# Performance work log

Hardware: AMD Instinct MI355X
Metric: run time of the kernel (lower is better)

## Reference

```python
import jax, jax.numpy as jnp
import numpy as np

V, E, H = 50000, 256, 512
BS, SEQ = 64, 200


def setup_inputs() -> dict:
    key = jax.random.key(0)
    ks = jax.random.split(key, 16)
    s = 0.05
    return {
        "input_idx": jax.random.randint(ks[0], (BS,), 0, V),
        "encoded": jax.random.normal(ks[1], (BS, SEQ, 2 * H), jnp.float32),
        "encoded_idx": jax.random.randint(ks[2], (BS, SEQ), 0, V),
        "prev_state": jax.random.normal(ks[3], (BS, H), jnp.float32),
        "weighted": jax.random.normal(ks[4], (BS, 1, 2 * H), jnp.float32),
        "order": 1,
        "embed_W": jax.random.normal(ks[5], (V, E), jnp.float32) * s,
        "Wih": jax.random.normal(ks[6], (3 * H, E + 2 * H), jnp.float32) * s,
        "Whh": jax.random.normal(ks[7], (3 * H, H), jnp.float32) * s,
        "bih": jax.random.normal(ks[8], (3 * H,), jnp.float32) * s,
        "bhh": jax.random.normal(ks[9], (3 * H,), jnp.float32) * s,
        "Ws_W": jax.random.normal(ks[10], (H, 2 * H), jnp.float32) * s,
        "Ws_b": jax.random.normal(ks[11], (H,), jnp.float32) * s,
        "Wo_W": jax.random.normal(ks[12], (V, H), jnp.float32) * s,
        "Wo_b": jax.random.normal(ks[13], (V,), jnp.float32) * s,
        "Wc_W": jax.random.normal(ks[14], (H, 2 * H), jnp.float32) * s,
        "Wc_b": jax.random.normal(ks[15], (H,), jnp.float32) * s,
    }


def reference(input_idx, encoded, encoded_idx, prev_state, weighted, order,
              embed_W, Wih, Whh, bih, bhh, Ws_W, Ws_b, Wo_W, Wo_b, Wc_W, Wc_b):
    bs, seq, _ = encoded.shape
    hidden = Ws_W.shape[0]
    vocab = Wo_W.shape[0]

    if order == 0:
        prev_state = encoded[:, 1] @ Ws_W.T + Ws_b            # [bs, H]
        weighted = jnp.zeros((bs, 1, 2 * hidden), encoded.dtype)

    # GRU single step (batch_first, seq len 1)
    x = jnp.concatenate([embed_W[input_idx], weighted[:, 0, :]], axis=1)  # [bs, E+2H]
    gi = x @ Wih.T + bih                                       # [bs, 3H]
    gh = prev_state @ Whh.T + bhh                              # [bs, 3H]
    i_r, i_z, i_n = jnp.split(gi, 3, axis=1)
    h_r, h_z, h_n = jnp.split(gh, 3, axis=1)
    r = jax.nn.sigmoid(i_r + h_r)
    z = jax.nn.sigmoid(i_z + h_z)
    n = jnp.tanh(i_n + r * h_n)
    state = (1.0 - z) * n + z * prev_state                     # [bs, H]

    # generate and copy scores
    score_g = state @ Wo_W.T + Wo_b                            # [bs, V]
    sc = jnp.tanh(encoded @ Wc_W.T + Wc_b)                     # [bs, seq, H]
    score_c = jnp.einsum('bsh,bh->bs', sc, state)              # [bs, seq]
    enc_mask = jnp.where(encoded_idx == 0, -1000.0, 0.0).astype(score_c.dtype)
    score_c = jnp.tanh(score_c + enc_mask)

    probs = jax.nn.softmax(jnp.concatenate([score_g, score_c], axis=1), axis=1)
    prob_g = probs[:, :vocab]                                  # [bs, V]
    prob_c = probs[:, vocab:]                                  # [bs, seq]

    # scatter-add copy probs into vocab slots
    prob_c_to_g = jnp.zeros((bs, vocab), probs.dtype).at[
        jnp.arange(bs)[:, None], encoded_idx].add(prob_c)
    out = (prob_g + prob_c_to_g)[:, None, :]                   # [bs, 1, V]

    # selective-read attention over positions matching input token
    m = (encoded_idx == input_idx[:, None]).astype(encoded.dtype)  # [bs, seq]
    ssum = m.sum(axis=1, keepdims=True)
    m = jnp.where(ssum > 1, m / ssum, m)
    attn = (prob_c * m)[:, None, :]                            # [bs, 1, seq]
    weighted_out = attn @ encoded                              # [bs, 1, 2H]

    return out, state, weighted_out
```

## Files before the change

kernel.cpp:

```cpp
#include <hip/hip_runtime.h>

#define V 50000
#define E_DIM 256
#define H_DIM 512
#define H2 1024
#define G3 1536
#define BSZ 64
#define SEQ 200
#define KX 1280
#define MROWS 12800
#define NBLK_WO 782

#define XBF_OFF   0
#define H0_OFF    40960
#define H0BF_OFF  73728
#define GI_OFF    90112
#define GH_OFF    188416
#define STBF_OFF  286720
#define WCBF_OFF  303104
#define SC_OFF    565248
#define REDG_OFF  616448
#define RED_OFF   716544
#define ENCBF_OFF 716672

#define OUT_STATE 3200000
#define OUT_W     3232768

typedef __attribute__((ext_vector_type(8))) short bf16x8;
typedef __attribute__((ext_vector_type(4))) float f32x4;

__device__ __forceinline__ float sigmf(float x) { return 1.f / (1.f + __expf(-x)); }

__device__ __forceinline__ ushort f2bf(float f) {
  uint u = __float_as_uint(f);
  uint r = (u + 0x7FFFu + ((u >> 16) & 1u)) >> 16;
  return (ushort)r;
}

__device__ __forceinline__ float tanhfast(float x) {
  float xc = fminf(15.f, fmaxf(-15.f, x));
  float e = __expf(2.f * xc);
  return (e - 1.f) * __builtin_amdgcn_rcpf(e + 1.f);
}

__device__ __forceinline__ bf16x8 cvt8(float4 a, float4 b) {
  union { bf16x8 v; uint u[4]; } r;
  asm("v_cvt_pk_bf16_f32 %0, %1, %2" : "=v"(r.u[0]) : "v"(a.x), "v"(a.y));
  asm("v_cvt_pk_bf16_f32 %0, %1, %2" : "=v"(r.u[1]) : "v"(a.z), "v"(a.w));
  asm("v_cvt_pk_bf16_f32 %0, %1, %2" : "=v"(r.u[2]) : "v"(b.x), "v"(b.y));
  asm("v_cvt_pk_bf16_f32 %0, %1, %2" : "=v"(r.u[3]) : "v"(b.z), "v"(b.w));
  return r.v;
}

__device__ __forceinline__ void gload16(const void* g, void* l) {
  __builtin_amdgcn_global_load_lds(
      (__attribute__((address_space(1))) void*)(g),
      (__attribute__((address_space(3))) void*)(l), 16, 0, 0);
}

__global__ void kprep(const float* __restrict__ Wc_W, ushort* __restrict__ Wc_bf,
                      const float* __restrict__ encoded, ushort* __restrict__ enc_bf,
                      const int* __restrict__ input_idx,
                      const float* __restrict__ prev_state, const float* __restrict__ weighted,
                      const int* __restrict__ order_p, const float* __restrict__ embed_W,
                      const float* __restrict__ Ws_W, const float* __restrict__ Ws_b,
                      ushort* __restrict__ x_bf, float* __restrict__ h0,
                      ushort* __restrict__ h0_bf) {
  int bid = blockIdx.x, tid = threadIdx.x;
  if (bid < 512) {
    int i = bid * 256 + tid;
    float4 v = ((const float4*)Wc_W)[i];
    ushort4 o;
    o.x = f2bf(v.x); o.y = f2bf(v.y); o.z = f2bf(v.z); o.w = f2bf(v.w);
    ((ushort4*)Wc_bf)[i] = o;
    return;
  }
  if (bid < 3712) {
    int base = (bid - 512) * 1024;
#pragma unroll
    for (int j = 0; j < 4; ++j) {
      int i = base + j * 256 + tid;
      float4 v = ((const float4*)encoded)[i];
      ushort4 o;
      o.x = f2bf(v.x); o.y = f2bf(v.y); o.z = f2bf(v.z); o.w = f2bf(v.w);
      ((ushort4*)enc_bf)[i] = o;
    }
    return;
  }
  int b = bid - 3712;
  int order = order_p[0];
  int idx = input_idx[b];
  x_bf[b * KX + tid] = f2bf(embed_W[(size_t)idx * E_DIM + tid]);
  if (order != 0) {
    for (int j = tid; j < H2; j += 256) x_bf[b * KX + E_DIM + j] = f2bf(weighted[b * H2 + j]);
    for (int j = tid; j < H_DIM; j += 256) {
      float v = prev_state[b * H_DIM + j];
      h0[b * H_DIM + j] = v;
      h0_bf[b * H_DIM + j] = f2bf(v);
    }
  } else {
    for (int j = tid; j < H2; j += 256) x_bf[b * KX + E_DIM + j] = 0;
    const float* er = encoded + ((size_t)b * SEQ + 1) * H2;
    for (int j = tid; j < H_DIM; j += 256) {
      float acc = Ws_b[j];
      const float* wr = Ws_W + (size_t)j * H2;
      for (int k = 0; k < H2; ++k) acc = fmaf(er[k], wr[k], acc);
      h0[b * H_DIM + j] = acc;
      h0_bf[b * H_DIM + j] = f2bf(acc);
    }
  }
}

__device__ __forceinline__ void gemm_small(const ushort* __restrict__ Abf,
                                           const float* __restrict__ W,
                                           const float* __restrict__ bias,
                                           float* __restrict__ out, int N, int kdim,
                                           int bid) {
  int tid = threadIdx.x;
  int lane = tid & 63, wv = tid >> 6;
  int l15 = lane & 15, lg = lane >> 4;
  int n0 = (bid * 4 + wv) * 16;
  int col = n0 + l15;
  bool valid = col < N;
  int colc = valid ? col : N - 1;
  f32x4 acc[4];
#pragma unroll
  for (int mt = 0; mt < 4; ++mt) acc[mt] = (f32x4){0.f, 0.f, 0.f, 0.f};
  const float* wrow = W + (size_t)colc * kdim + lg * 8;
  const ushort* arow = Abf + (size_t)l15 * kdim + lg * 8;
#pragma unroll 4
  for (int k0 = 0; k0 < kdim; k0 += 32) {
    float4 w0 = *(const float4*)(wrow + k0);
    float4 w1 = *(const float4*)(wrow + k0 + 4);
    bf16x8 bf = cvt8(w0, w1);
#pragma unroll
    for (int mt = 0; mt < 4; ++mt) {
      bf16x8 af = *(const bf16x8*)(arow + (size_t)mt * 16 * kdim + k0);
      acc[mt] = __builtin_amdgcn_mfma_f32_16x16x32_bf16(af, bf, acc[mt], 0, 0, 0);
    }
  }
  float bv = bias[colc];
  if (valid) {
#pragma unroll
    for (int mt = 0; mt < 4; ++mt)
#pragma unroll
      for (int r = 0; r < 4; ++r)
        out[(size_t)(mt * 16 + lg * 4 + r) * N + col] = acc[mt][r] + bv;
  }
}

__global__ __launch_bounds__(256) void mfma_gates(const ushort* __restrict__ x_bf,
                                                  const float* __restrict__ Wih,
                                                  const float* __restrict__ bih,
                                                  const ushort* __restrict__ h0_bf,
                                                  const float* __restrict__ Whh,
                                                  const float* __restrict__ bhh,
                                                  float* __restrict__ gi, float* __restrict__ gh) {
  if (blockIdx.y == 0)
    gemm_small(x_bf, Wih, bih, gi, G3, KX, blockIdx.x);
  else
    gemm_small(h0_bf, Whh, bhh, gh, G3, H_DIM, blockIdx.x);
}

__global__ void k2_gru(const float* __restrict__ gi, const float* __restrict__ gh,
                       const float* __restrict__ h0, float* __restrict__ state_out,
                       ushort* __restrict__ state_bf) {
  int b = blockIdx.x, j = threadIdx.x;
  float ir = gi[b * G3 + j], iz = gi[b * G3 + H_DIM + j], inn = gi[b * G3 + 2 * H_DIM + j];
  float hr = gh[b * G3 + j], hz = gh[b * G3 + H_DIM + j], hn = gh[b * G3 + 2 * H_DIM + j];
  float r = sigmf(ir + hr);
  float z = sigmf(iz + hz);
  float n = tanhf(inn + r * hn);
  float st = (1.f - z) * n + z * h0[b * H_DIM + j];
  state_out[b * H_DIM + j] = st;
  state_bf[b * H_DIM + j] = f2bf(st);
}

__global__ __launch_bounds__(256) void wo_stage(const ushort* __restrict__ state_bf,
                                                const float* __restrict__ Wo_W,
                                                const float* __restrict__ Wo_b,
                                                float* __restrict__ out,
                                                float* __restrict__ redg) {
  __shared__ char ldsA[32768];
  __shared__ char ldsW[2][4][2048];
  __shared__ float sm[4][32], ss[4][32];
  int tid = threadIdx.x, lane = tid & 63, wv = tid >> 6;
  int l15 = lane & 15, lg = lane >> 4;
  int bid = blockIdx.x, yh = blockIdx.y;
  int col0 = bid * 64 + wv * 16 + l15;
  bool v0ok = col0 < V;
  int cc0 = v0ok ? col0 : V - 1;
  const float* s0 = Wo_W + (size_t)cc0 * H_DIM + lg * 8;

#pragma unroll
  for (int j = 0; j < 8; ++j) {
    int slot = wv * 8 + j;
    int mf = slot >> 4, it = slot & 15;
    gload16(state_bf + (size_t)(yh * 32 + mf * 16 + l15) * H_DIM + it * 32 + lg * 8,
            ldsA + slot * 1024);
  }
  {
    char* d_ = &ldsW[0][wv][0];
    gload16(s0, d_);
    gload16(s0 + 4, d_ + 1024);
  }
  __syncthreads();

  f32x4 acc[2];
  acc[0] = (f32x4){0.f, 0.f, 0.f, 0.f};
  acc[1] = (f32x4){0.f, 0.f, 0.f, 0.f};

#pragma unroll 1
  for (int it = 0; it < 16; ++it) {
    int cur = it & 1;
    if (it < 15) {
      char* d_ = &ldsW[cur ^ 1][wv][0];
      gload16(s0 + (it + 1) * 32, d_);
      gload16(s0 + (it + 1) * 32 + 4, d_ + 1024);
      asm volatile("s_waitcnt vmcnt(2)" ::: "memory");
    } else {
      asm volatile("s_waitcnt vmcnt(0)" ::: "memory");
    }
    const char* wb = &ldsW[cur][wv][0];
    float4 w00 = *(const float4*)(wb + lane * 16);
    float4 w01 = *(const float4*)(wb + 1024 + lane * 16);
    bf16x8 wf0 = cvt8(w00, w01);
    bf16x8 af0 = *(const bf16x8*)(ldsA + (0 * 16 + it) * 1024 + lane * 16);
    bf16x8 af1 = *(const bf16x8*)(ldsA + (1 * 16 + it) * 1024 + lane * 16);
    acc[0] = __builtin_amdgcn_mfma_f32_16x16x32_bf16(af0, wf0, acc[0], 0, 0, 0);
    acc[1] = __builtin_amdgcn_mfma_f32_16x16x32_bf16(af1, wf0, acc[1], 0, 0, 0);
  }

  float bv0 = Wo_b[cc0];
#pragma unroll
  for (int mf = 0; mf < 2; ++mf)
#pragma unroll
    for (int r = 0; r < 4; ++r) {
      size_t row = (size_t)(yh * 32 + mf * 16 + lg * 4 + r) * V;
      if (v0ok) out[row + col0] = acc[mf][r] + bv0;
    }
#pragma unroll
  for (int mf = 0; mf < 2; ++mf)
#pragma unroll
    for (int r = 0; r < 4; ++r) {
      float a0 = v0ok ? acc[mf][r] + bv0 : -1e30f;
      float mx = a0;
#pragma unroll
      for (int off = 1; off < 16; off <<= 1) mx = fmaxf(mx, __shfl_xor(mx, off, 64));
      float e = v0ok ? __expf(a0 - mx) : 0.f;
#pragma unroll
      for (int off = 1; off < 16; off <<= 1) e += __shfl_xor(e, off, 64);
      if (l15 == 0) {
        sm[wv][mf * 16 + lg * 4 + r] = mx;
        ss[wv][mf * 16 + lg * 4 + r] = e;
      }
    }
  __syncthreads();
  if (tid < 32) {
    float M = -1e30f, S = 0.f;
#pragma unroll
    for (int w = 0; w < 4; ++w) {
      float m2 = sm[w][tid], s2 = ss[w][tid];
      float mn = fmaxf(M, m2);
      S = S * __expf(M - mn) + s2 * __expf(m2 - mn);
      M = mn;
    }
    redg[((size_t)(yh * 32 + tid) * NBLK_WO + bid) * 2] = M;
    redg[((size_t)(yh * 32 + tid) * NBLK_WO + bid) * 2 + 1] = S;
  }
}

__global__ __launch_bounds__(256) void k4_mfma9(const ushort* __restrict__ enc_bf,
                                                const ushort* __restrict__ Wc_bf,
                                                const float* __restrict__ Wc_b,
                                                const float* __restrict__ state,
                                                float* __restrict__ scpart) {
  __shared__ char lds[2][24576];
  __shared__ float sred[4][64];
  int tid = threadIdx.x, lane = tid & 63, wv = tid >> 6;
  int l15 = lane & 15, lg = lane >> 4;
  int bid = blockIdx.x;
  int mtile = bid >> 2, ntile = bid & 3;
  int m0 = mtile * 64, n0 = ntile * 128;

  const ushort* asrc = enc_bf + (size_t)(m0 + wv * 16 + l15) * H2 + lg * 8;
  const ushort* bsrc0 = Wc_bf + (size_t)(n0 + (wv * 2 + 0) * 16 + l15) * H2 + lg * 8;
  const ushort* bsrc1 = Wc_bf + (size_t)(n0 + (wv * 2 + 1) * 16 + l15) * H2 + lg * 8;

  f32x4 acc[4][2];
#pragma unroll
  for (int mf = 0; mf < 4; ++mf)
#pragma unroll
    for (int nf = 0; nf < 2; ++nf) acc[mf][nf] = (f32x4){0.f, 0.f, 0.f, 0.f};

#define STG(buf, it) do {                                              \
    char* d_ = &lds[buf][0];                                           \
    gload16(asrc + (it) * 64,       d_ + (wv * 2 + 0) * 1024);         \
    gload16(asrc + (it) * 64 + 32,  d_ + (wv * 2 + 1) * 1024);         \
    gload16(bsrc0 + (it) * 64,      d_ + 8192 + (wv * 4 + 0) * 1024);  \
    gload16(bsrc0 + (it) * 64 + 32, d_ + 8192 + (wv * 4 + 1) * 1024);  \
    gload16(bsrc1 + (it) * 64,      d_ + 8192 + (wv * 4 + 2) * 1024);  \
    gload16(bsrc1 + (it) * 64 + 32, d_ + 8192 + (wv * 4 + 3) * 1024);  \
  } while (0)

  STG(0, 0);
  __syncthreads();
#pragma unroll 1
  for (int it = 0; it < 16; ++it) {
    int cur = it & 1;
    if (it < 15) STG(cur ^ 1, it + 1);
    const char* base = &lds[cur][0];
#pragma unroll
    for (int ks = 0; ks < 2; ++ks) {
      bf16x8 b0 = *(const bf16x8*)(base + 8192 + (wv * 4 + ks) * 1024 + lane * 16);
      bf16x8 b1 = *(const bf16x8*)(base + 8192 + (wv * 4 + 2 + ks) * 1024 + lane * 16);
#pragma unroll
      for (int mf = 0; mf < 4; ++mf) {
        bf16x8 a = *(const bf16x8*)(base + (mf * 2 + ks) * 1024 + lane * 16);
        acc[mf][0] = __builtin_amdgcn_mfma_f32_16x16x32_bf16(a, b0, acc[mf][0], 0, 0, 0);
        acc[mf][1] = __builtin_amdgcn_mfma_f32_16x16x32_bf16(a, b1, acc[mf][1], 0, 0, 0);
      }
    }
    __syncthreads();
  }
#undef STG

  float pv[4][4];
#pragma unroll
  for (int mf = 0; mf < 4; ++mf)
#pragma unroll
    for (int r = 0; r < 4; ++r) pv[mf][r] = 0.f;
#pragma unroll
  for (int nfl = 0; nfl < 2; ++nfl) {
    int n = n0 + (wv * 2 + nfl) * 16 + l15;
    float bias = Wc_b[n];
#pragma unroll
    for (int mf = 0; mf < 4; ++mf) {
      int mrow = m0 + mf * 16 + lg * 4;
#pragma unroll
      for (int r = 0; r < 4; ++r) {
        int b = (mrow + r) / SEQ;
        pv[mf][r] += tanhfast(acc[mf][nfl][r] + bias) * state[b * H_DIM + n];
      }
    }
  }
#pragma unroll
  for (int off = 1; off < 16; off <<= 1)
#pragma unroll
    for (int mf = 0; mf < 4; ++mf)
#pragma unroll
      for (int r = 0; r < 4; ++r) pv[mf][r] += __shfl_xor(pv[mf][r], off, 64);
  if (l15 == 0) {
#pragma unroll
    for (int mf = 0; mf < 4; ++mf)
#pragma unroll
      for (int r = 0; r < 4; ++r) sred[wv][mf * 16 + lg * 4 + r] = pv[mf][r];
  }
  __syncthreads();
  if (tid < 64) {
    float s = sred[0][tid] + sred[1][tid] + sred[2][tid] + sred[3][tid];
    scpart[(size_t)ntile * MROWS + m0 + tid] = s;
  }
}

__global__ void kred(const float* __restrict__ redg, const float* __restrict__ scpart,
                     const int* __restrict__ eidx, float* __restrict__ red) {
  int b = blockIdx.x, tid = threadIdx.x;
  float m = -1e30f, s = 0.f;
  for (int i = tid; i < NBLK_WO; i += 256) {
    float m2 = redg[((size_t)b * NBLK_WO + i) * 2];
    float s2 = redg[((size_t)b * NBLK_WO + i) * 2 + 1];
    float mn = fmaxf(m, m2);
    s = s * __expf(m - mn) + s2 * __expf(m2 - mn);
    m = mn;
  }
  for (int i = tid; i < SEQ; i += 256) {
    int idx = b * SEQ + i;
    int ei = eidx[idx];
    float scv = scpart[idx] + scpart[MROWS + idx] + scpart[2 * MROWS + idx] +
                scpart[3 * MROWS + idx];
    float sc = tanhf(scv + (ei == 0 ? -1000.f : 0.f));
    float mn = fmaxf(m, sc);
    s = s * __expf(m - mn) + __expf(sc - mn);
    m = mn;
  }
  __shared__ float ms[256], ssh[256];
  ms[tid] = m; ssh[tid] = s;
  __syncthreads();
  for (int off = 128; off > 0; off >>= 1) {
    if (tid < off) {
      float m2 = ms[tid + off], s2 = ssh[tid + off];
      float mn = fmaxf(ms[tid], m2);
      ssh[tid] = ssh[tid] * __expf(ms[tid] - mn) + s2 * __expf(m2 - mn);
      ms[tid] = mn;
    }
    __syncthreads();
  }
  if (tid == 0) {
    red[b * 2] = ms[0];
    red[b * 2 + 1] = ssh[0];
  }
}

__global__ void k7_probs(float* __restrict__ sg, const float* __restrict__ red) {
  int i = blockIdx.x * 256 + threadIdx.x;
  int b = i / 12500;
  float mm = red[b * 2], rd = 1.f / red[b * 2 + 1];
  float4* p = (float4*)sg;
  float4 v = p[i];
  v.x = __expf(v.x - mm) * rd;
  v.y = __expf(v.y - mm) * rd;
  v.z = __expf(v.z - mm) * rd;
  v.w = __expf(v.w - mm) * rd;
  p[i] = v;
}

__global__ void k8_copy(const float* __restrict__ scpart, const int* __restrict__ eidx,
                        const int* __restrict__ input_idx, const float* __restrict__ red,
                        const float* __restrict__ encoded, float* __restrict__ out,
                        float* __restrict__ wout) {
  int b = blockIdx.x, tid = threadIdx.x;
  __shared__ float att_s[SEQ];
  __shared__ int cnt_s[256];
  float mm = red[b * 2], rd = 1.f / red[b * 2 + 1];
  int inp = input_idx[b];
  int cnt = 0;
  for (int s = tid; s < SEQ; s += 256) {
    int idx = b * SEQ + s;
    int ei = eidx[idx];
    float scv = scpart[idx] + scpart[MROWS + idx] + scpart[2 * MROWS + idx] +
                scpart[3 * MROWS + idx];
    float sc = tanhf(scv + (ei == 0 ? -1000.f : 0.f));
    float p = __expf(sc - mm) * rd;
    bool mt = (ei == inp);
    att_s[s] = mt ? p : 0.f;
    cnt += mt ? 1 : 0;
    atomicAdd(&out[(size_t)b * V + ei], p);
  }
  cnt_s[tid] = cnt;
  __syncthreads();
  for (int off = 128; off > 0; off >>= 1) {
    if (tid < off) cnt_s[tid] += cnt_s[tid + off];
    __syncthreads();
  }
  int c = cnt_s[0];
  float scale = (c > 1) ? 1.f / (float)c : 1.f;
  float w0 = 0, w1 = 0, w2 = 0, w3 = 0;
  for (int s = 0; s < SEQ; ++s) {
    float a = att_s[s];
    if (a != 0.f) {
      const float* er = encoded + ((size_t)b * SEQ + s) * H2;
      w0 += a * er[tid];
      w1 += a * er[tid + 256];
      w2 += a * er[tid + 512];
      w3 += a * er[tid + 768];
    }
  }
  wout[b * H2 + tid] = w0 * scale;
  wout[b * H2 + tid + 256] = w1 * scale;
  wout[b * H2 + tid + 512] = w2 * scale;
  wout[b * H2 + tid + 768] = w3 * scale;
}

extern "C" void kernel_launch(void* const* d_in, const int* in_sizes, int n_in,
                              void* d_out, int out_size, void* d_ws, size_t ws_size,
                              hipStream_t stream) {
  const int* input_idx = (const int*)d_in[0];
  const float* encoded = (const float*)d_in[1];
  const int* encoded_idx = (const int*)d_in[2];
  const float* prev_state = (const float*)d_in[3];
  const float* weighted = (const float*)d_in[4];
  const int* order_p = (const int*)d_in[5];
  const float* embed_W = (const float*)d_in[6];
  const float* Wih = (const float*)d_in[7];
  const float* Whh = (const float*)d_in[8];
  const float* bih = (const float*)d_in[9];
  const float* bhh = (const float*)d_in[10];
  const float* Ws_W = (const float*)d_in[11];
  const float* Ws_b = (const float*)d_in[12];
  const float* Wo_W = (const float*)d_in[13];
  const float* Wo_b = (const float*)d_in[14];
  const float* Wc_W = (const float*)d_in[15];
  const float* Wc_b = (const float*)d_in[16];

  float* ws = (float*)d_ws;
  float* out = (float*)d_out;
  ushort* x_bf = (ushort*)(ws + XBF_OFF);
  float* h0 = ws + H0_OFF;
  ushort* h0_bf = (ushort*)(ws + H0BF_OFF);
  float* gi = ws + GI_OFF;
  float* gh = ws + GH_OFF;
  ushort* state_bf = (ushort*)(ws + STBF_OFF);
  ushort* Wc_bf = (ushort*)(ws + WCBF_OFF);
  float* scpart = ws + SC_OFF;
  float* redg = ws + REDG_OFF;
  float* red = ws + RED_OFF;
  ushort* enc_bf = (ushort*)(ws + ENCBF_OFF);
  float* state = out + OUT_STATE;
  float* wout = out + OUT_W;

  kprep<<<3776, 256, 0, stream>>>(Wc_W, Wc_bf, encoded, enc_bf, input_idx, prev_state,
                                  weighted, order_p, embed_W, Ws_W, Ws_b, x_bf, h0, h0_bf);
  mfma_gates<<<dim3(24, 2), 256, 0, stream>>>(x_bf, Wih, bih, h0_bf, Whh, bhh, gi, gh);
  k2_gru<<<64, 512, 0, stream>>>(gi, gh, h0, state, state_bf);
  wo_stage<<<dim3(NBLK_WO, 2), 256, 0, stream>>>(state_bf, Wo_W, Wo_b, out, redg);
  k4_mfma9<<<800, 256, 0, stream>>>(enc_bf, Wc_bf, Wc_b, state, scpart);
  kred<<<64, 256, 0, stream>>>(redg, scpart, encoded_idx, red);
  k7_probs<<<3125, 256, 0, stream>>>(out, red);
  k8_copy<<<64, 256, 0, stream>>>(scpart, encoded_idx, input_idx, red, encoded, out, wout);
}
```

Before: 180.6 us.

## Cover all 64 batch rows per Wo block to read Wo_W once

The Wo projection grid drops its second dimension, so each block now computes all 64 batch rows (four MFMA row tiles) for its 64 vocab columns instead of 32 rows over two blocks. This halves global reads of the fp32 Wo_W matrix, which the old split loaded twice. The shared buffers merge into one 80 KB array with the softmax partials aliased over the weight staging area. In exchange, LDS per block rises and the grid halves, so fewer blocks may be resident per CU.

```diff
diff --git a/kernel.cpp b/kernel.cpp
--- a/kernel.cpp
+++ b/kernel.cpp
@@ -176,74 +176,78 @@
   state_bf[b * H_DIM + j] = f2bf(st);
 }
 
-__global__ __launch_bounds__(256) void wo_stage(const ushort* __restrict__ state_bf,
-                                                const float* __restrict__ Wo_W,
-                                                const float* __restrict__ Wo_b,
-                                                float* __restrict__ out,
-                                                float* __restrict__ redg) {
-  __shared__ char ldsA[32768];
-  __shared__ char ldsW[2][4][2048];
-  __shared__ float sm[4][32], ss[4][32];
+__global__ __launch_bounds__(256, 2) void wo_stage(const ushort* __restrict__ state_bf,
+                                                   const float* __restrict__ Wo_W,
+                                                   const float* __restrict__ Wo_b,
+                                                   float* __restrict__ out,
+                                                   float* __restrict__ redg) {
+  __shared__ char shmem[81920];
   int tid = threadIdx.x, lane = tid & 63, wv = tid >> 6;
   int l15 = lane & 15, lg = lane >> 4;
-  int bid = blockIdx.x, yh = blockIdx.y;
+  int bid = blockIdx.x;
   int col0 = bid * 64 + wv * 16 + l15;
   bool v0ok = col0 < V;
   int cc0 = v0ok ? col0 : V - 1;
   const float* s0 = Wo_W + (size_t)cc0 * H_DIM + lg * 8;
 
 #pragma unroll
-  for (int j = 0; j < 8; ++j) {
-    int slot = wv * 8 + j;
+  for (int j = 0; j < 16; ++j) {
+    int slot = wv * 16 + j;
     int mf = slot >> 4, it = slot & 15;
-    gload16(state_bf + (size_t)(yh * 32 + mf * 16 + l15) * H_DIM + it * 32 + lg * 8,
-            ldsA + slot * 1024);
+    gload16(state_bf + (size_t)(mf * 16 + l15) * H_DIM + it * 32 + lg * 8,
+            shmem + slot * 1024);
   }
   {
-    char* d_ = &ldsW[0][wv][0];
+    char* d_ = shmem + 65536 + wv * 2048;
     gload16(s0, d_);
     gload16(s0 + 4, d_ + 1024);
   }
   __syncthreads();
 
-  f32x4 acc[2];
-  acc[0] = (f32x4){0.f, 0.f, 0.f, 0.f};
-  acc[1] = (f32x4){0.f, 0.f, 0.f, 0.f};
+  f32x4 acc[4];
+#pragma unroll
+  for (int mt = 0; mt < 4; ++mt) acc[mt] = (f32x4){0.f, 0.f, 0.f, 0.f};
 
 #pragma unroll 1
   for (int it = 0; it < 16; ++it) {
     int cur = it & 1;
     if (it < 15) {
-      char* d_ = &ldsW[cur ^ 1][wv][0];
+      char* d_ = shmem + 65536 + (cur ^ 1) * 8192 + wv * 2048;
       gload16(s0 + (it + 1) * 32, d_);
       gload16(s0 + (it + 1) * 32 + 4, d_ + 1024);
       asm volatile("s_waitcnt vmcnt(2)" ::: "memory");
     } else {
       asm volatile("s_waitcnt vmcnt(0)" ::: "memory");
     }
-    const char* wb = &ldsW[cur][wv][0];
+    const char* wb = shmem + 65536 + cur * 8192 + wv * 2048;
     float4 w00 = *(const float4*)(wb + lane * 16);
     float4 w01 = *(const float4*)(wb + 1024 + lane * 16);
     bf16x8 wf0 = cvt8(w00, w01);
-    bf16x8 af0 = *(const bf16x8*)(ldsA + (0 * 16 + it) * 1024 + lane * 16);
-    bf16x8 af1 = *(const bf16x8*)(ldsA + (1 * 16 + it) * 1024 + lane * 16);
+    bf16x8 af0 = *(const bf16x8*)(shmem + (0 * 16 + it) * 1024 + lane * 16);
+    bf16x8 af1 = *(const bf16x8*)(shmem + (1 * 16 + it) * 1024 + lane * 16);
+    bf16x8 af2 = *(const bf16x8*)(shmem + (2 * 16 + it) * 1024 + lane * 16);
+    bf16x8 af3 = *(const bf16x8*)(shmem + (3 * 16 + it) * 1024 + lane * 16);
     acc[0] = __builtin_amdgcn_mfma_f32_16x16x32_bf16(af0, wf0, acc[0], 0, 0, 0);
     acc[1] = __builtin_amdgcn_mfma_f32_16x16x32_bf16(af1, wf0, acc[1], 0, 0, 0);
+    acc[2] = __builtin_amdgcn_mfma_f32_16x16x32_bf16(af2, wf0, acc[2], 0, 0, 0);
+    acc[3] = __builtin_amdgcn_mfma_f32_16x16x32_bf16(af3, wf0, acc[3], 0, 0, 0);
   }
 
   float bv0 = Wo_b[cc0];
 #pragma unroll
-  for (int mf = 0; mf < 2; ++mf)
+  for (int mt = 0; mt < 4; ++mt)
 #pragma unroll
     for (int r = 0; r < 4; ++r) {
-      size_t row = (size_t)(yh * 32 + mf * 16 + lg * 4 + r) * V;
-      if (v0ok) out[row + col0] = acc[mf][r] + bv0;
-    }
-#pragma unroll
-  for (int mf = 0; mf < 2; ++mf)
+      size_t row = (size_t)(mt * 16 + lg * 4 + r) * V;
+      if (v0ok) out[row + col0] = acc[mt][r] + bv0;
+    }
+  float* smw = (float*)(shmem + 65536 + wv * 2048);
+  float* ssw = smw + 64;
+#pragma unroll
+  for (int mt = 0; mt < 4; ++mt)
 #pragma unroll
     for (int r = 0; r < 4; ++r) {
-      float a0 = v0ok ? acc[mf][r] + bv0 : -1e30f;
+      float a0 = v0ok ? acc[mt][r] + bv0 : -1e30f;
       float mx = a0;
 #pragma unroll
       for (int off = 1; off < 16; off <<= 1) mx = fmaxf(mx, __shfl_xor(mx, off, 64));
@@ -251,22 +255,23 @@
 #pragma unroll
       for (int off = 1; off < 16; off <<= 1) e += __shfl_xor(e, off, 64);
       if (l15 == 0) {
-        sm[wv][mf * 16 + lg * 4 + r] = mx;
-        ss[wv][mf * 16 + lg * 4 + r] = e;
+        smw[mt * 16 + lg * 4 + r] = mx;
+        ssw[mt * 16 + lg * 4 + r] = e;
       }
     }
   __syncthreads();
-  if (tid < 32) {
+  if (tid < 64) {
     float M = -1e30f, S = 0.f;
 #pragma unroll
     for (int w = 0; w < 4; ++w) {
-      float m2 = sm[w][tid], s2 = ss[w][tid];
+      const float* smx = (const float*)(shmem + 65536 + w * 2048);
+      float m2 = smx[tid], s2 = smx[64 + tid];
       float mn = fmaxf(M, m2);
       S = S * __expf(M - mn) + s2 * __expf(m2 - mn);
       M = mn;
     }
-    redg[((size_t)(yh * 32 + tid) * NBLK_WO + bid) * 2] = M;
-    redg[((size_t)(yh * 32 + tid) * NBLK_WO + bid) * 2 + 1] = S;
+    redg[((size_t)tid * NBLK_WO + bid) * 2] = M;
+    redg[((size_t)tid * NBLK_WO + bid) * 2 + 1] = S;
   }
 }
 
@@ -503,7 +508,7 @@
                                   weighted, order_p, embed_W, Ws_W, Ws_b, x_bf, h0, h0_bf);
   mfma_gates<<<dim3(24, 2), 256, 0, stream>>>(x_bf, Wih, bih, h0_bf, Whh, bhh, gi, gh);
   k2_gru<<<64, 512, 0, stream>>>(gi, gh, h0, state, state_bf);
-  wo_stage<<<dim3(NBLK_WO, 2), 256, 0, stream>>>(state_bf, Wo_W, Wo_b, out, redg);
+  wo_stage<<<NBLK_WO, 256, 0, stream>>>(state_bf, Wo_W, Wo_b, out, redg);
   k4_mfma9<<<800, 256, 0, stream>>>(enc_bf, Wc_bf, Wc_b, state, scpart);
   kred<<<64, 256, 0, stream>>>(redg, scpart, encoded_idx, red);
   k7_probs<<<3125, 256, 0, stream>>>(out, red);
```

Result: faster. 164.0 us (-9.2%).
